# Kernel tuning notes

Measured on AMD Instinct MI355X. Metric: run time of the kernel, lower is better.

## Reference

```python
import jax, jax.numpy as jnp
import numpy as np

BN_EPS = 1e-5


def setup_inputs() -> dict:
    key = jax.random.key(0)
    k1, k2 = jax.random.split(key)
    B, IN, OUT = 16384, 2048, 2048
    x = jax.random.normal(k1, (B, IN), dtype=jnp.float32)
    weight = jax.random.normal(k2, (OUT, IN), dtype=jnp.float32) * 0.05
    gamma = jnp.ones((OUT,), dtype=jnp.float32)
    beta = jnp.zeros((OUT,), dtype=jnp.float32)
    return {"x": x, "weight": weight, "gamma": gamma, "beta": beta}


def reference(x, weight, gamma, beta):
    # Deterministic binarization: sign(w) in {-1, +1} (0 maps to +1)
    w_bin = jnp.where(weight >= 0, 1.0, -1.0).astype(weight.dtype)
    # Linear (no bias): y = x @ W_bin^T  -> [B, OUT]
    y = jnp.einsum("bi,oi->bo", x, w_bin)
    # BatchNorm1d, training mode: biased batch statistics over batch dim
    mean = jnp.mean(y, axis=0)
    var = jnp.mean(jnp.square(y - mean), axis=0)
    y = (y - mean) * (gamma * jax.lax.rsqrt(var + BN_EPS)) + beta
    # ReLU activation
    return jax.nn.relu(y)
```

## Files before the change

### kernel.cpp

```cpp
#include <hip/hip_runtime.h>
#include <stdint.h>

#define B_DIM   16384
#define IN_DIM  2048
#define OUT_DIM 2048
#define BN_EPS  1e-5f

typedef int    i32x4 __attribute__((ext_vector_type(4)));
typedef unsigned short u16x4 __attribute__((ext_vector_type(4)));


__device__ __forceinline__ unsigned short f2bf_rne(float f) {
    unsigned u = __builtin_bit_cast(unsigned, f);
    return (unsigned short)((u + 0x7fffu + ((u >> 16) & 1u)) >> 16);
}
__device__ __forceinline__ float bf2f(unsigned short h) {
    unsigned u = ((unsigned)h) << 16;
    return __builtin_bit_cast(float, u);
}

__device__ __forceinline__ void gl_lds16(const void* g, void* l) {
    __builtin_amdgcn_global_load_lds(
        (const __attribute__((address_space(1))) unsigned int*)g,
        (__attribute__((address_space(3))) unsigned int*)l,
        16, 0, 0);
}

__device__ __forceinline__ int pack4(float a, float b, float c, float d, float inv) {
    int q0 = (int)rintf(a * inv) & 255;
    int q1 = (int)rintf(b * inv) & 255;
    int q2 = (int)rintf(c * inv) & 255;
    int q3 = (int)rintf(d * inv) & 255;
    return q0 | (q1 << 8) | (q2 << 16) | (q3 << 24);
}

__global__ __launch_bounds__(256) void quantize_x_kernel(
        const float4* __restrict__ x4, int* __restrict__ xq,
        float* __restrict__ scales) {
    __shared__ float wmax[4];
    const int row = blockIdx.x;
    const int t = threadIdx.x;
    const float4* xr = x4 + (size_t)row * 512;
    float4 a = xr[t];
    float4 b = xr[t + 256];
    float m = fmaxf(fmaxf(fabsf(a.x), fabsf(a.y)), fmaxf(fabsf(a.z), fabsf(a.w)));
    m = fmaxf(m, fmaxf(fmaxf(fabsf(b.x), fabsf(b.y)), fmaxf(fabsf(b.z), fabsf(b.w))));
#pragma unroll
    for (int off = 32; off >= 1; off >>= 1) m = fmaxf(m, __shfl_xor(m, off));
    if ((t & 63) == 0) wmax[t >> 6] = m;
    __syncthreads();
    m = fmaxf(fmaxf(wmax[0], wmax[1]), fmaxf(wmax[2], wmax[3]));
    m = fmaxf(m, 1e-20f);
    const float inv = 127.0f / m;
    if (t == 0) scales[row] = m * (1.0f / 127.0f);
    int* xo = xq + (size_t)row * 512;
    xo[t]       = pack4(a.x, a.y, a.z, a.w, inv);
    xo[t + 256] = pack4(b.x, b.y, b.z, b.w, inv);
}

__global__ __launch_bounds__(256) void convert_w_kernel(
        const float4* __restrict__ w, int* __restrict__ wq,
        float4* __restrict__ stats ) {
    int id = blockIdx.x * 256 + threadIdx.x;
    if (id < 1024) stats[id] = make_float4(0.f, 0.f, 0.f, 0.f);
    float4 a = w[id];
    int b0 = (a.x < 0.f) ? 0xFF : 0x01;
    int b1 = (a.y < 0.f) ? 0xFF : 0x01;
    int b2 = (a.z < 0.f) ? 0xFF : 0x01;
    int b3 = (a.w < 0.f) ? 0xFF : 0x01;
    wq[id] = b0 | (b1 << 8) | (b2 << 16) | (b3 << 24);
}

__global__ __launch_bounds__(512, 4) void gemm_bn_kernel(
        const char* __restrict__ A, const char* __restrict__ Bw,
        const float* __restrict__ scales,
        unsigned short* __restrict__ Yb,
        float* __restrict__ colsum, float* __restrict__ colsumsq) {
    __shared__ __align__(16) char smem[2 * 24576];

    const int tid  = threadIdx.x;
    const int wave = tid >> 6;
    const int lane = tid & 63;
    const int wm = wave >> 1;
    const int wn = wave & 1;
    const int lr = lane & 15;
    const int lq = lane >> 4;

    const int b  = blockIdx.x;
    const int lb = (b & 7) * 128 + (b >> 3);
    const int bm = (lb >> 4) * 256;
    const int bn = (lb & 15) * 128;

    const int swz16 = (((tid & 3) ^ ((tid >> 3) & 3)) << 4);
    const char* gA0 = A  + (size_t)(bm + (tid >> 2)) * IN_DIM + swz16;
    const char* gA1 = gA0 + (size_t)128 * IN_DIM;
    const char* gB0 = Bw + (size_t)(bn + (tid >> 2)) * IN_DIM + swz16;
    const int ldst = tid << 4;

    const int ps   = ((lq ^ ((lr >> 1) & 3)) << 4);
    const int aoff = (wm * 64 + lr) * 64 + ps;
    const int boff = 16384 + (wn * 64 + lr) * 64 + ps;

    i32x4 acc[4][4];
#pragma unroll
    for (int i = 0; i < 4; ++i)
#pragma unroll
        for (int j = 0; j < 4; ++j) {
            i32x4 z = {0, 0, 0, 0};
            acc[i][j] = z;
        }

#define VM_WAIT(N) asm volatile("s_waitcnt vmcnt(" #N ")" ::: "memory")
#define BAR()      __builtin_amdgcn_s_barrier()
#define STAGE(buf_, k_) do {                                   \
    char* d = smem + (buf_) * 24576;                           \
    gl_lds16(gA0 + (k_), d + ldst);                            \
    gl_lds16(gA1 + (k_), d + 8192 + ldst);                     \
    gl_lds16(gB0 + (k_), d + 16384 + ldst);                    \
} while (0)

    STAGE(0, 0);
    STAGE(1, 64);
    VM_WAIT(3);
    BAR();

    const int NT = IN_DIM / 64;
#pragma unroll
    for (int t = 0; t < NT; ++t) {
        const int cur = t & 1;
        const char* Sb = smem + cur * 24576;
        i32x4 av[4], bv[4];
#pragma unroll
        for (int i = 0; i < 4; ++i)
            av[i] = *(const i32x4*)(Sb + aoff + i * 1024);
#pragma unroll
        for (int j = 0; j < 4; ++j)
            bv[j] = *(const i32x4*)(Sb + boff + j * 1024);

        __builtin_amdgcn_s_setprio(1);
#pragma unroll
        for (int i = 0; i < 4; ++i)
#pragma unroll
            for (int j = 0; j < 4; ++j)
                acc[i][j] = __builtin_amdgcn_mfma_i32_16x16x64_i8(
                    av[i], bv[j], acc[i][j], 0, 0, 0);
        __builtin_amdgcn_s_setprio(0);

        if (t + 2 < NT) {
            BAR();
            STAGE(cur, (size_t)(t + 2) * 64);
            VM_WAIT(3);
            BAR();
        } else if (t + 1 < NT) {
            VM_WAIT(0);
            BAR();
        }
    }

#undef STAGE
#undef VM_WAIT
#undef BAR

    float colS[4], colQ[4];
#pragma unroll
    for (int j = 0; j < 4; ++j) { colS[j] = 0.f; colQ[j] = 0.f; }

#pragma unroll
    for (int i = 0; i < 4; ++i) {
        const int row0 = bm + wm * 64 + i * 16 + lq * 4;
        float sc[4];
#pragma unroll
        for (int r = 0; r < 4; ++r) sc[r] = scales[row0 + r];
#pragma unroll
        for (int r = 0; r < 4; ++r) {
            size_t base = (size_t)(row0 + r) * OUT_DIM + bn + wn * 64 + lr;
#pragma unroll
            for (int j = 0; j < 4; ++j) {
                float v = (float)acc[i][j][r] * sc[r];
                Yb[base + j * 16] = f2bf_rne(v);
                colS[j] += v;
                colQ[j] += v * v;
            }
        }
    }

#pragma unroll
    for (int j = 0; j < 4; ++j) {
        float s = colS[j], q = colQ[j];
        s += __shfl_xor(s, 16); s += __shfl_xor(s, 32);
        q += __shfl_xor(q, 16); q += __shfl_xor(q, 32);
        if (lq == 0) {
            int col = bn + wn * 64 + j * 16 + lr;
            atomicAdd(&colsum[col], s);
            atomicAdd(&colsumsq[col], q);
        }
    }
}

__global__ __launch_bounds__(256) void finalize_kernel(
        const float* __restrict__ colsum, const float* __restrict__ colsumsq,
        const float* __restrict__ gamma, const float* __restrict__ beta,
        float* __restrict__ scale, float* __restrict__ bias) {
    int n = blockIdx.x * 256 + threadIdx.x;
    if (n < OUT_DIM) {
        const float inv = 1.f / (float)B_DIM;
        float mean = colsum[n] * inv;
        float var  = colsumsq[n] * inv - mean * mean;
        float sc   = gamma[n] * rsqrtf(var + BN_EPS);
        scale[n] = sc;
        bias[n]  = beta[n] - mean * sc;
    }
}

__global__ __launch_bounds__(256) void bn_relu_bf16_kernel(
        const u16x4* __restrict__ yb, float4* __restrict__ out,
        const float4* __restrict__ scale4, const float4* __restrict__ bias4) {
    int base = blockIdx.x * 512 + threadIdx.x;
#pragma unroll
    for (int p = 0; p < 2; ++p) {
        int id = base + p * 256;
        int c4 = id & (OUT_DIM / 4 - 1);
        u16x4 h = yb[id];
        float4 s = scale4[c4];
        float4 bb = bias4[c4];
        float4 v;
        v.x = fmaxf(fmaf(bf2f(h[0]), s.x, bb.x), 0.f);
        v.y = fmaxf(fmaf(bf2f(h[1]), s.y, bb.y), 0.f);
        v.z = fmaxf(fmaf(bf2f(h[2]), s.z, bb.z), 0.f);
        v.w = fmaxf(fmaf(bf2f(h[3]), s.w, bb.w), 0.f);
        out[id] = v;
    }
}

extern "C" void kernel_launch(void* const* d_in, const int* in_sizes, int n_in,
                              void* d_out, int out_size, void* d_ws, size_t ws_size,
                              hipStream_t stream) {
    const float* x     = (const float*)d_in[0];
    const float* w     = (const float*)d_in[1];
    const float* gamma = (const float*)d_in[2];
    const float* beta  = (const float*)d_in[3];
    float* out = (float*)d_out;

    char* ws = (char*)d_ws;
    const size_t XQ_OFF = 0;
    const size_t WQ_OFF = XQ_OFF + (size_t)B_DIM * IN_DIM;
    const size_t YB_OFF = WQ_OFF + (size_t)OUT_DIM * IN_DIM;
    const size_t ST_OFF = YB_OFF + (size_t)B_DIM * OUT_DIM * 2;
    const size_t SC_OFF = ST_OFF + 8192 * 4;

    char* xq = ws + XQ_OFF;
    char* wq = ws + WQ_OFF;
    unsigned short* yb = (unsigned short*)(ws + YB_OFF);
    float* colsum   = (float*)(ws + ST_OFF);
    float* colsumsq = colsum + 2048;
    float* scale    = colsum + 4096;
    float* bias     = colsum + 6144;
    float* scales   = (float*)(ws + SC_OFF);

    quantize_x_kernel<<<B_DIM, 256, 0, stream>>>(
        (const float4*)x, (int*)xq, scales);
    convert_w_kernel<<<4096, 256, 0, stream>>>(
        (const float4*)w, (int*)wq, (float4*)colsum);
    gemm_bn_kernel<<<1024, 512, 0, stream>>>(
        xq, wq, scales, yb, colsum, colsumsq);
    finalize_kernel<<<8, 256, 0, stream>>>(
        colsum, colsumsq, gamma, beta, scale, bias);
    bn_relu_bf16_kernel<<<16384, 256, 0, stream>>>(
        (const u16x4*)yb, (float4*)out, (const float4*)scale,
        (const float4*)bias);
}
```

Measured before the change: 335.4 us.

## Enlarge int8 GEMM tile to 256x256 with 128-deep K stages

The int8 GEMM block tile grows from 256x128 to 256x256, and each wave now computes a 128x64 sub-tile with 32 accumulators. K staging doubles to 128 bytes per stage, using 128 KB of double-buffered LDS and a 3-bit XOR swizzle. The grid is halved to 512 blocks. The aim is more MFMA work per LDS byte and per global load, cutting memory traffic per output. The cost is higher register pressure, occupancy limited to about one block per CU, and fewer blocks to spread across CUs.

```diff
diff --git a/kernel.cpp b/kernel.cpp
--- a/kernel.cpp
+++ b/kernel.cpp
@@ -71,39 +71,39 @@
     wq[id] = b0 | (b1 << 8) | (b2 << 16) | (b3 << 24);
 }
 
-__global__ __launch_bounds__(512, 4) void gemm_bn_kernel(
+__global__ __launch_bounds__(512, 2) void gemm_bn_kernel(
         const char* __restrict__ A, const char* __restrict__ Bw,
         const float* __restrict__ scales,
         unsigned short* __restrict__ Yb,
         float* __restrict__ colsum, float* __restrict__ colsumsq) {
-    __shared__ __align__(16) char smem[2 * 24576];
+    __shared__ __align__(16) char smem[131072];
 
     const int tid  = threadIdx.x;
     const int wave = tid >> 6;
     const int lane = tid & 63;
-    const int wm = wave >> 1;
-    const int wn = wave & 1;
+    const int wm = wave >> 2;
+    const int wn = wave & 3;
     const int lr = lane & 15;
     const int lq = lane >> 4;
 
     const int b  = blockIdx.x;
-    const int lb = (b & 7) * 128 + (b >> 3);
-    const int bm = (lb >> 4) * 256;
-    const int bn = (lb & 15) * 128;
-
-    const int swz16 = (((tid & 3) ^ ((tid >> 3) & 3)) << 4);
-    const char* gA0 = A  + (size_t)(bm + (tid >> 2)) * IN_DIM + swz16;
-    const char* gA1 = gA0 + (size_t)128 * IN_DIM;
-    const char* gB0 = Bw + (size_t)(bn + (tid >> 2)) * IN_DIM + swz16;
+    const int lb = (b & 7) * 64 + (b >> 3);
+    const int bm = (lb >> 3) * 256;
+    const int bn = (lb & 7) * 256;
+
+    const int swz16 = (((tid & 7) ^ ((tid >> 3) & 7)) << 4);
+    const char* gA = A  + (size_t)(bm + (tid >> 3)) * IN_DIM + swz16;
+    const char* gB = Bw + (size_t)(bn + (tid >> 3)) * IN_DIM + swz16;
     const int ldst = tid << 4;
 
-    const int ps   = ((lq ^ ((lr >> 1) & 3)) << 4);
-    const int aoff = (wm * 64 + lr) * 64 + ps;
-    const int boff = 16384 + (wn * 64 + lr) * 64 + ps;
-
-    i32x4 acc[4][4];
-#pragma unroll
-    for (int i = 0; i < 4; ++i)
+    const int aRd = wm * 16384 + lr * 128;
+    const int bRd = 32768 + wn * 8192 + lr * 128;
+    const int sl0 = ((lq    ) ^ (lr & 7)) << 4;
+    const int sl1 = ((lq + 4) ^ (lr & 7)) << 4;
+
+    i32x4 acc[8][4];
+#pragma unroll
+    for (int i = 0; i < 8; ++i)
 #pragma unroll
         for (int j = 0; j < 4; ++j) {
             i32x4 z = {0, 0, 0, 0};
@@ -112,44 +112,66 @@
 
 #define VM_WAIT(N) asm volatile("s_waitcnt vmcnt(" #N ")" ::: "memory")
 #define BAR()      __builtin_amdgcn_s_barrier()
-#define STAGE(buf_, k_) do {                                   \
-    char* d = smem + (buf_) * 24576;                           \
-    gl_lds16(gA0 + (k_), d + ldst);                            \
-    gl_lds16(gA1 + (k_), d + 8192 + ldst);                     \
-    gl_lds16(gB0 + (k_), d + 16384 + ldst);                    \
+#define STAGE(buf_, k_) do {                                        \
+    char* d = smem + (buf_) * 65536;                                \
+    gl_lds16(gA + (k_)          , d + 0 * 8192 + ldst);             \
+    gl_lds16(gA + (k_) + 131072 , d + 1 * 8192 + ldst);             \
+    gl_lds16(gA + (k_) + 262144 , d + 2 * 8192 + ldst);             \
+    gl_lds16(gA + (k_) + 393216 , d + 3 * 8192 + ldst);             \
+    gl_lds16(gB + (k_)          , d + 32768 + 0 * 8192 + ldst);     \
+    gl_lds16(gB + (k_) + 131072 , d + 32768 + 1 * 8192 + ldst);     \
+    gl_lds16(gB + (k_) + 262144 , d + 32768 + 2 * 8192 + ldst);     \
+    gl_lds16(gB + (k_) + 393216 , d + 32768 + 3 * 8192 + ldst);     \
 } while (0)
 
     STAGE(0, 0);
-    STAGE(1, 64);
-    VM_WAIT(3);
+    STAGE(1, 128);
+    VM_WAIT(8);
     BAR();
 
-    const int NT = IN_DIM / 64;
-#pragma unroll
+    const int NT = IN_DIM / 128;
+#pragma unroll 2
     for (int t = 0; t < NT; ++t) {
-        const int cur = t & 1;
-        const char* Sb = smem + cur * 24576;
-        i32x4 av[4], bv[4];
-#pragma unroll
-        for (int i = 0; i < 4; ++i)
-            av[i] = *(const i32x4*)(Sb + aoff + i * 1024);
-#pragma unroll
-        for (int j = 0; j < 4; ++j)
-            bv[j] = *(const i32x4*)(Sb + boff + j * 1024);
-
-        __builtin_amdgcn_s_setprio(1);
-#pragma unroll
-        for (int i = 0; i < 4; ++i)
+        const char* Sb = smem + (t & 1) * 65536;
+        {
+            i32x4 av[8], bv[4];
+#pragma unroll
+            for (int i = 0; i < 8; ++i)
+                av[i] = *(const i32x4*)(Sb + aRd + i * 2048 + sl0);
 #pragma unroll
             for (int j = 0; j < 4; ++j)
-                acc[i][j] = __builtin_amdgcn_mfma_i32_16x16x64_i8(
-                    av[i], bv[j], acc[i][j], 0, 0, 0);
-        __builtin_amdgcn_s_setprio(0);
+                bv[j] = *(const i32x4*)(Sb + bRd + j * 2048 + sl0);
+            __builtin_amdgcn_s_setprio(1);
+#pragma unroll
+            for (int i = 0; i < 8; ++i)
+#pragma unroll
+                for (int j = 0; j < 4; ++j)
+                    acc[i][j] = __builtin_amdgcn_mfma_i32_16x16x64_i8(
+                        av[i], bv[j], acc[i][j], 0, 0, 0);
+            __builtin_amdgcn_s_setprio(0);
+        }
+        {
+            i32x4 av[8], bv[4];
+#pragma unroll
+            for (int i = 0; i < 8; ++i)
+                av[i] = *(const i32x4*)(Sb + aRd + i * 2048 + sl1);
+#pragma unroll
+            for (int j = 0; j < 4; ++j)
+                bv[j] = *(const i32x4*)(Sb + bRd + j * 2048 + sl1);
+            __builtin_amdgcn_s_setprio(1);
+#pragma unroll
+            for (int i = 0; i < 8; ++i)
+#pragma unroll
+                for (int j = 0; j < 4; ++j)
+                    acc[i][j] = __builtin_amdgcn_mfma_i32_16x16x64_i8(
+                        av[i], bv[j], acc[i][j], 0, 0, 0);
+            __builtin_amdgcn_s_setprio(0);
+        }
 
         if (t + 2 < NT) {
             BAR();
-            STAGE(cur, (size_t)(t + 2) * 64);
-            VM_WAIT(3);
+            STAGE(t & 1, (size_t)(t + 2) * 128);
+            VM_WAIT(8);
             BAR();
         } else if (t + 1 < NT) {
             VM_WAIT(0);
@@ -166,8 +188,8 @@
     for (int j = 0; j < 4; ++j) { colS[j] = 0.f; colQ[j] = 0.f; }
 
 #pragma unroll
-    for (int i = 0; i < 4; ++i) {
-        const int row0 = bm + wm * 64 + i * 16 + lq * 4;
+    for (int i = 0; i < 8; ++i) {
+        const int row0 = bm + wm * 128 + i * 16 + lq * 4;
         float sc[4];
 #pragma unroll
         for (int r = 0; r < 4; ++r) sc[r] = scales[row0 + r];
@@ -261,7 +283,7 @@
         (const float4*)x, (int*)xq, scales);
     convert_w_kernel<<<4096, 256, 0, stream>>>(
         (const float4*)w, (int*)wq, (float4*)colsum);
-    gemm_bn_kernel<<<1024, 512, 0, stream>>>(
+    gemm_bn_kernel<<<512, 512, 0, stream>>>(
         xq, wq, scales, yb, colsum, colsumsq);
     finalize_kernel<<<8, 256, 0, stream>>>(
         colsum, colsumsq, gamma, beta, scale, bias);
```

Measured after the change: 331.2 us. No clear change (-1.2%).

## Load A fragments directly to registers and stage only B in LDS

Applied to the files above, without the earlier changes.

The int8 GEMM now uses 256-thread blocks with 128x128 tiles and a K step of 128. Only the weight tile goes through LDS, with a wider XOR swizzle. Each wave loads its own A (activation) fragments from global memory straight into registers, double-buffered across the two K halves. This cuts LDS traffic and footprint and raises occupancy, at the cost of uncoalesced per-lane global loads of A and more A reloads from global, since the M tile is smaller.

```diff
diff --git a/kernel.cpp b/kernel.cpp
--- a/kernel.cpp
+++ b/kernel.cpp
@@ -71,12 +71,12 @@
     wq[id] = b0 | (b1 << 8) | (b2 << 16) | (b3 << 24);
 }
 
-__global__ __launch_bounds__(512, 4) void gemm_bn_kernel(
+__global__ __launch_bounds__(256, 3) void gemm_bn_kernel(
         const char* __restrict__ A, const char* __restrict__ Bw,
         const float* __restrict__ scales,
         unsigned short* __restrict__ Yb,
         float* __restrict__ colsum, float* __restrict__ colsumsq) {
-    __shared__ __align__(16) char smem[2 * 24576];
+    __shared__ __align__(16) char smem[2 * 16384];
 
     const int tid  = threadIdx.x;
     const int wave = tid >> 6;
@@ -86,20 +86,24 @@
     const int lr = lane & 15;
     const int lq = lane >> 4;
 
-    const int b  = blockIdx.x;
-    const int lb = (b & 7) * 128 + (b >> 3);
-    const int bm = (lb >> 4) * 256;
-    const int bn = (lb & 15) * 128;
-
-    const int swz16 = (((tid & 3) ^ ((tid >> 3) & 3)) << 4);
-    const char* gA0 = A  + (size_t)(bm + (tid >> 2)) * IN_DIM + swz16;
-    const char* gA1 = gA0 + (size_t)128 * IN_DIM;
-    const char* gB0 = Bw + (size_t)(bn + (tid >> 2)) * IN_DIM + swz16;
+    const int b   = blockIdx.x;
+    const int xcd = b & 7;
+    const int l   = b >> 3;
+    const int bn  = (xcd * 2 + (l & 1)) * 128;
+    const int bm  = (l >> 1) * 128;
+
+    const char* gA0 = A + (size_t)(bm + wm * 64 + lr) * IN_DIM + lq * 16;
+    const char* gA1 = gA0 + 1 * 16 * IN_DIM;
+    const char* gA2 = gA0 + 2 * 16 * IN_DIM;
+    const char* gA3 = gA0 + 3 * 16 * IN_DIM;
+
+    const int swz16 = (((tid & 7) ^ ((tid >> 3) & 7)) << 4);
+    const char* gB = Bw + (size_t)(bn + (tid >> 3)) * IN_DIM + swz16;
     const int ldst = tid << 4;
 
-    const int ps   = ((lq ^ ((lr >> 1) & 3)) << 4);
-    const int aoff = (wm * 64 + lr) * 64 + ps;
-    const int boff = 16384 + (wn * 64 + lr) * 64 + ps;
+    const int bRd = (wn * 64 + lr) * 128;
+    const int sl0 = ((lq    ) ^ (lr & 7)) << 4;
+    const int sl1 = ((lq + 4) ^ (lr & 7)) << 4;
 
     i32x4 acc[4][4];
 #pragma unroll
@@ -112,52 +116,80 @@
 
 #define VM_WAIT(N) asm volatile("s_waitcnt vmcnt(" #N ")" ::: "memory")
 #define BAR()      __builtin_amdgcn_s_barrier()
-#define STAGE(buf_, k_) do {                                   \
-    char* d = smem + (buf_) * 24576;                           \
-    gl_lds16(gA0 + (k_), d + ldst);                            \
-    gl_lds16(gA1 + (k_), d + 8192 + ldst);                     \
-    gl_lds16(gB0 + (k_), d + 16384 + ldst);                    \
+#define STAGEB(buf_, koff_) do {                                    \
+    char* d = smem + (buf_) * 16384;                                \
+    gl_lds16(gB + (koff_)          , d + 0 * 4096 + ldst);          \
+    gl_lds16(gB + (koff_) +  65536 , d + 1 * 4096 + ldst);          \
+    gl_lds16(gB + (koff_) + 131072 , d + 2 * 4096 + ldst);          \
+    gl_lds16(gB + (koff_) + 196608 , d + 3 * 4096 + ldst);          \
 } while (0)
 
-    STAGE(0, 0);
-    STAGE(1, 64);
-    VM_WAIT(3);
+    i32x4 avX[4], avY[4];
+
+    avX[0] = *(const i32x4*)(gA0);
+    avX[1] = *(const i32x4*)(gA1);
+    avX[2] = *(const i32x4*)(gA2);
+    avX[3] = *(const i32x4*)(gA3);
+    STAGEB(0, 0);
+    STAGEB(1, 128);
+    VM_WAIT(4);
     BAR();
 
-    const int NT = IN_DIM / 64;
+    const int NT = IN_DIM / 128;
 #pragma unroll
     for (int t = 0; t < NT; ++t) {
-        const int cur = t & 1;
-        const char* Sb = smem + cur * 24576;
-        i32x4 av[4], bv[4];
-#pragma unroll
-        for (int i = 0; i < 4; ++i)
-            av[i] = *(const i32x4*)(Sb + aoff + i * 1024);
-#pragma unroll
-        for (int j = 0; j < 4; ++j)
-            bv[j] = *(const i32x4*)(Sb + boff + j * 1024);
-
-        __builtin_amdgcn_s_setprio(1);
-#pragma unroll
-        for (int i = 0; i < 4; ++i)
+        const char* Bb = smem + (t & 1) * 16384;
+        avY[0] = *(const i32x4*)(gA0 + t * 128 + 64);
+        avY[1] = *(const i32x4*)(gA1 + t * 128 + 64);
+        avY[2] = *(const i32x4*)(gA2 + t * 128 + 64);
+        avY[3] = *(const i32x4*)(gA3 + t * 128 + 64);
+        {
+            i32x4 bv[4];
 #pragma unroll
             for (int j = 0; j < 4; ++j)
-                acc[i][j] = __builtin_amdgcn_mfma_i32_16x16x64_i8(
-                    av[i], bv[j], acc[i][j], 0, 0, 0);
-        __builtin_amdgcn_s_setprio(0);
-
+                bv[j] = *(const i32x4*)(Bb + bRd + j * 2048 + sl0);
+            __builtin_amdgcn_s_setprio(1);
+#pragma unroll
+            for (int i = 0; i < 4; ++i)
+#pragma unroll
+                for (int j = 0; j < 4; ++j)
+                    acc[i][j] = __builtin_amdgcn_mfma_i32_16x16x64_i8(
+                        avX[i], bv[j], acc[i][j], 0, 0, 0);
+            __builtin_amdgcn_s_setprio(0);
+        }
+        if (t + 1 < NT) {
+            avX[0] = *(const i32x4*)(gA0 + (t + 1) * 128);
+            avX[1] = *(const i32x4*)(gA1 + (t + 1) * 128);
+            avX[2] = *(const i32x4*)(gA2 + (t + 1) * 128);
+            avX[3] = *(const i32x4*)(gA3 + (t + 1) * 128);
+        }
+        {
+            i32x4 bv[4];
+#pragma unroll
+            for (int j = 0; j < 4; ++j)
+                bv[j] = *(const i32x4*)(Bb + bRd + j * 2048 + sl1);
+            __builtin_amdgcn_s_setprio(1);
+#pragma unroll
+            for (int i = 0; i < 4; ++i)
+#pragma unroll
+                for (int j = 0; j < 4; ++j)
+                    acc[i][j] = __builtin_amdgcn_mfma_i32_16x16x64_i8(
+                        avY[i], bv[j], acc[i][j], 0, 0, 0);
+            __builtin_amdgcn_s_setprio(0);
+        }
         if (t + 2 < NT) {
             BAR();
-            STAGE(cur, (size_t)(t + 2) * 64);
-            VM_WAIT(3);
+            STAGEB(t & 1, (t + 2) * 128);
+            VM_WAIT(4);
             BAR();
         } else if (t + 1 < NT) {
+            BAR();
             VM_WAIT(0);
             BAR();
         }
     }
 
-#undef STAGE
+#undef STAGEB
 #undef VM_WAIT
 #undef BAR
 
@@ -261,7 +293,7 @@
         (const float4*)x, (int*)xq, scales);
     convert_w_kernel<<<4096, 256, 0, stream>>>(
         (const float4*)w, (int*)wq, (float4*)colsum);
-    gemm_bn_kernel<<<1024, 512, 0, stream>>>(
+    gemm_bn_kernel<<<2048, 256, 0, stream>>>(
         xq, wq, scales, yb, colsum, colsumsq);
     finalize_kernel<<<8, 256, 0, stream>>>(
         colsum, colsumsq, gamma, beta, scale, bias);
```

Measured after the change: 400.4 us. 19.4% more time.
